# Kernel optimization log

Measured on AMD Instinct MI355X. Metric: run time of the kernel, lower is better.

## Reference

```python
import jax, jax.numpy as jnp
import numpy as np
from jax import lax

NUM_CLS = 58

def _bsign(a):
    # BNN sign: +1 for a >= 0, -1 otherwise
    return jnp.where(a >= 0, 1.0, -1.0).astype(a.dtype)

def _conv(x, w, stride=1):
    return lax.conv_general_dilated(
        x, w, window_strides=(stride, stride), padding='VALID',
        dimension_numbers=('NCHW', 'OIHW', 'NCHW'))

def _binconv(x, w):
    # BinaryConv2d: binarize activations and weights via sign, then conv
    return _conv(_bsign(x), _bsign(w))

def _maxpool(x, k=2, s=2):
    return lax.reduce_window(x, -jnp.inf, lax.max,
                             (1, 1, k, k), (1, 1, s, s), 'VALID')

def setup_inputs() -> dict:
    key = jax.random.key(0)
    ks = jax.random.split(key, 7)
    B = 1024
    x = jax.random.normal(ks[0], (B, 3, 32, 32), dtype=jnp.float32)
    w0 = jax.random.normal(ks[1], (128, 3, 3, 3), dtype=jnp.float32) * 0.1   # float conv
    w1 = jax.random.normal(ks[2], (128, 128, 3, 3), dtype=jnp.float32) * 0.1 # binary conv
    w2 = jax.random.normal(ks[3], (128, 128, 3, 3), dtype=jnp.float32) * 0.1 # binary conv
    w3 = jax.random.normal(ks[4], (128, 128, 3, 3), dtype=jnp.float32) * 0.1 # binary conv
    w4 = jax.random.normal(ks[5], (128, 128, 1, 1), dtype=jnp.float32) * 0.1 # binary 1x1
    w5 = jax.random.normal(ks[6], (NUM_CLS, 128, 1, 1), dtype=jnp.float32) * 0.1  # float 1x1
    return {'x': x, 'w0': w0, 'w1': w1, 'w2': w2, 'w3': w3, 'w4': w4, 'w5': w5}

def reference(x, w0, w1, w2, w3, w4, w5):
    # features
    h = _conv(x, w0)            # [B,128,30,30]
    h = _maxpool(h, 2, 2)       # [B,128,15,15]
    h = _binconv(h, w1)         # [B,128,13,13]
    h = _maxpool(h, 2, 2)       # [B,128,6,6]
    h = _binconv(h, w2)         # [B,128,4,4]
    h = _maxpool(h, 2, 1)       # [B,128,3,3]
    # classifier
    h = _binconv(h, w3)         # [B,128,1,1]
    h = _binconv(h, w4)         # [B,128,1,1]
    h = jax.nn.relu(h)
    h = _conv(h, w5)            # [B,58,1,1]
    return jax.nn.softmax(h, axis=1)
```

## Files before the change

kernel.cpp:

```cpp
#include <hip/hip_runtime.h>
#include <cmath>

#define NUM_CLS 58

typedef _Float16 v8h __attribute__((ext_vector_type(8)));
typedef float v4f __attribute__((ext_vector_type(4)));
union HU { v8h h; uint4 u; };

__global__ __launch_bounds__(256) void prep_all(
    const float* __restrict__ w0, const float* __restrict__ w1,
    const float* __restrict__ w2, const float* __restrict__ w3,
    const float* __restrict__ w4,
    unsigned long long* __restrict__ wb1, unsigned long long* __restrict__ wb2,
    unsigned long long* __restrict__ wb3, unsigned long long* __restrict__ wb4,
    _Float16* __restrict__ bsig, _Float16* __restrict__ babs) {
    int id = blockIdx.x, tid = threadIdx.x;
    int lane = tid & 63, wv = tid >> 6;
    if (id < 384) {
        int layer = id >> 7, oc = id & 127;
        const float* w = layer == 0 ? w1 : (layer == 1 ? w2 : w3);
        unsigned long long* o = layer == 0 ? wb1 : (layer == 1 ? wb2 : wb3);
        __shared__ float s[1152];
        const float* base = w + (size_t)oc * 1152;
        for (int i = tid; i < 1152; i += 256) s[i] = base[i];
        __syncthreads();
        for (int k = wv; k < 9; k += 4) {
            unsigned long long b0 = __ballot(s[lane * 9 + k] >= 0.f);
            unsigned long long b1 = __ballot(s[(lane + 64) * 9 + k] >= 0.f);
            if (lane == 0) { o[(oc * 9 + k) * 2] = b0; o[(oc * 9 + k) * 2 + 1] = b1; }
        }
    } else if (id < 416) {
        int oc = (id - 384) * 4 + wv;
        unsigned long long b0 = __ballot(w4[oc * 128 + lane] >= 0.f);
        unsigned long long b1 = __ballot(w4[oc * 128 + lane + 64] >= 0.f);
        if (lane == 0) { wb4[oc * 2] = b0; wb4[oc * 2 + 1] = b1; }
    } else {
        int nt = (id - 416) * 4 + wv;
        int n = nt * 16 + (lane & 15);
        int k0 = (lane >> 4) * 8;
#pragma unroll
        for (int j = 0; j < 8; j++) {
            int k = k0 + j;
            float v = (k < 27) ? w0[n * 27 + k] : 0.f;
            bsig[(nt * 64 + lane) * 8 + j] = (_Float16)v;
            babs[(nt * 64 + lane) * 8 + j] = (_Float16)fabsf(v);
        }
    }
}

__global__ __launch_bounds__(256, 4) void fused_net(
    const float* __restrict__ x, const float* __restrict__ w0,
    const _Float16* __restrict__ bsigG, const _Float16* __restrict__ babsG,
    const unsigned long long* __restrict__ wb1, const unsigned long long* __restrict__ wb2,
    const unsigned long long* __restrict__ wb3, const unsigned long long* __restrict__ wb4,
    const float* __restrict__ w5, float* __restrict__ out) {
    __shared__ _Float16 xh[3172];
    __shared__ uint4 bfrag[512];
    __shared__ uint4 bfraga[512];
    __shared__ alignas(16) unsigned long long bits1[450];
    __shared__ alignas(16) unsigned long long bits2[72];
    __shared__ unsigned long long bits3[18];
    __shared__ unsigned long long bits4[2];
    __shared__ float r_s[128];
    __shared__ float l_s[NUM_CLS];
    __shared__ float e_s[NUM_CLS];
    __shared__ unsigned int qcnt;
    __shared__ unsigned int queue[256];

    int b = blockIdx.x;
    int tid = threadIdx.x;
    int lane = tid & 63, wave = tid >> 6;
    const float* xb = x + (size_t)b * 3072;

    {
        for (int i = tid; i < 3072; i += 256) {
            int c = i >> 10, rem = i & 1023;
            xh[c * 1057 + (rem >> 5) * 33 + (rem & 31)] = (_Float16)xb[i];
        }
        const uint4* bs4 = (const uint4*)bsigG;
        const uint4* ba4 = (const uint4*)babsG;
        for (int i = tid; i < 512; i += 256) { bfrag[i] = bs4[i]; bfraga[i] = ba4[i]; }
        if (tid == 0) qcnt = 0;

        int k0 = (lane >> 4) * 8;
        int offj[8];
#pragma unroll
        for (int j = 0; j < 8; j++) {
            int k = k0 + j;
            int c = k / 9, r = (k % 9) / 3, q = k % 3;
            offj[j] = c * 1057 + r * 33 + q;
        }
        unsigned short* b1u16 = (unsigned short*)bits1;
        __syncthreads();

        for (int mt = wave; mt < 57; mt += 4) {
            int mg = mt * 16 + (lane & 15);
            int me = mg < 900 ? mg : 899;
            int p = me >> 2, win = me & 3;
            int py = p / 15, px = p - py * 15;
            int base = (py * 2 + (win >> 1)) * 33 + px * 2 + (win & 1);
            v8h a;
#pragma unroll
            for (int j = 0; j < 8; j++)
                a[j] = (k0 + j < 27) ? xh[base + offj[j]] : (_Float16)0.f;
            HU ua; ua.h = a;
            ua.u.x &= 0x7FFF7FFFu; ua.u.y &= 0x7FFF7FFFu;
            ua.u.z &= 0x7FFF7FFFu; ua.u.w &= 0x7FFF7FFFu;
            int myp = mt * 4 + (lane >> 4);
#pragma unroll
            for (int nt = 0; nt < 8; nt++) {
                HU bs; bs.u = bfrag[nt * 64 + lane];
                HU ba; ba.u = bfraga[nt * 64 + lane];
                v4f s  = __builtin_amdgcn_mfma_f32_16x16x32_f16(a,    bs.h, (v4f){0.f,0.f,0.f,0.f}, 0, 0, 0);
                v4f sa = __builtin_amdgcn_mfma_f32_16x16x32_f16(ua.h, ba.h, (v4f){0.f,0.f,0.f,0.f}, 0, 0, 0);
                float bd0 = fmaf(sa[0], 1.1e-3f, 1e-5f);
                float bd1 = fmaf(sa[1], 1.1e-3f, 1e-5f);
                float bd2 = fmaf(sa[2], 1.1e-3f, 1e-5f);
                float bd3 = fmaf(sa[3], 1.1e-3f, 1e-5f);
                unsigned long long mkpos =
                    __ballot(s[0] >= bd0) | __ballot(s[1] >= bd1) |
                    __ballot(s[2] >= bd2) | __ballot(s[3] >= bd3);
                unsigned long long mkunc =
                    (__ballot(fabsf(s[0]) < bd0) | __ballot(fabsf(s[1]) < bd1) |
                     __ballot(fabsf(s[2]) < bd2) | __ballot(fabsf(s[3]) < bd3)) & ~mkpos;
                if ((lane & 15) == 0 && myp < 225)
                    b1u16[myp * 8 + nt] = (unsigned short)(mkpos >> (lane & 48));
                if (__builtin_expect(mkunc != 0ull, 0)) {
                    if (((mkunc >> lane) & 1ull) && myp < 225) {
                        unsigned int qi = atomicAdd(&qcnt, 1u);
                        if (qi < 256) queue[qi] = (unsigned)myp | ((unsigned)(nt * 16 + (lane & 15)) << 8);
                    }
                }
            }
        }
        __syncthreads();
        unsigned int nq = qcnt < 256u ? qcnt : 256u;
        for (unsigned int i = tid; i < nq; i += 256) {
            unsigned int e = queue[i];
            int p = e & 255; int oc = (e >> 8) & 255;
            int py = p / 15, px = p - py * 15;
            bool pos = false;
#pragma unroll
            for (int win = 0; win < 4; win++) {
                int base = (py * 2 + (win >> 1)) * 32 + px * 2 + (win & 1);
                double sd = 0.0;
#pragma unroll
                for (int k = 0; k < 27; k++) {
                    int c = k / 9, r = (k % 9) / 3, q = k % 3;
                    sd += (double)xb[base + c * 1024 + r * 32 + q] * (double)w0[oc * 27 + k];
                }
                pos |= (sd >= 0.0);
            }
            if (pos) atomicOr(&bits1[p * 2 + (oc >> 6)], 1ull << (oc & 63));
        }
    }
    __syncthreads();

    int wave2 = tid >> 6, half = wave2 & 1, pair = wave2 >> 1;
    int oc = half * 64 + lane;

    {
        unsigned long long wr[18];
#pragma unroll
        for (int j = 0; j < 18; j++) wr[j] = wb1[oc * 18 + j];
        const ulonglong2* b1v = (const ulonglong2*)bits1;
        for (int p = pair; p < 36; p += 2) {
            int py = p / 6, px = p % 6;
            int P0 = 0, P1 = 0, P2 = 0, P3 = 0;
#pragma unroll
            for (int yy = 0; yy < 4; yy++) {
                int rb = (2 * py + yy) * 15 + 2 * px;
                ulonglong2 q0 = b1v[rb];
                ulonglong2 q1 = b1v[rb + 1];
                ulonglong2 q2 = b1v[rb + 2];
                ulonglong2 q3 = b1v[rb + 3];
#pragma unroll
                for (int dy = 0; dy < 2; dy++) {
                    int ky = yy - dy;
                    if (ky < 0 || ky > 2) continue;
#pragma unroll
                    for (int kx = 0; kx < 3; kx++) {
                        ulonglong2 qa = kx == 0 ? q0 : (kx == 1 ? q1 : q2);
                        ulonglong2 qb = kx == 0 ? q1 : (kx == 1 ? q2 : q3);
                        int d0 = __popcll(qa.x ^ wr[(ky * 3 + kx) * 2]) +
                                 __popcll(qa.y ^ wr[(ky * 3 + kx) * 2 + 1]);
                        int d1 = __popcll(qb.x ^ wr[(ky * 3 + kx) * 2]) +
                                 __popcll(qb.y ^ wr[(ky * 3 + kx) * 2 + 1]);
                        if (dy == 0) { P0 += d0; P1 += d1; }
                        else         { P2 += d0; P3 += d1; }
                    }
                }
            }
            unsigned long long m = __ballot(P0 <= 576) | __ballot(P1 <= 576) |
                                   __ballot(P2 <= 576) | __ballot(P3 <= 576);
            if (lane == 0) bits2[p * 2 + half] = m;
        }
    }
    __syncthreads();

    {
        unsigned long long wr[18];
#pragma unroll
        for (int j = 0; j < 18; j++) wr[j] = wb2[oc * 18 + j];
        const ulonglong2* b2v = (const ulonglong2*)bits2;
        for (int p = pair; p < 9; p += 2) {
            int py = p / 3, px = p % 3;
            int P4[4];
#pragma unroll
            for (int dy = 0; dy < 2; dy++)
#pragma unroll
                for (int dx = 0; dx < 2; dx++) {
                    int P = 0;
#pragma unroll
                    for (int ky = 0; ky < 3; ky++)
#pragma unroll
                        for (int kx = 0; kx < 3; kx++) {
                            ulonglong2 q = b2v[(py + dy + ky) * 6 + (px + dx + kx)];
                            P += __popcll(q.x ^ wr[(ky * 3 + kx) * 2]);
                            P += __popcll(q.y ^ wr[(ky * 3 + kx) * 2 + 1]);
                        }
                    P4[dy * 2 + dx] = P;
                }
            unsigned long long m = __ballot(P4[0] <= 576) | __ballot(P4[1] <= 576) |
                                   __ballot(P4[2] <= 576) | __ballot(P4[3] <= 576);
            if (lane == 0) bits3[p * 2 + half] = m;
        }
    }
    __syncthreads();

    if (tid < 128) {
        int P = 0;
#pragma unroll
        for (int k = 0; k < 9; k++) {
            P += __popcll(bits3[k * 2] ^ wb3[tid * 18 + k * 2]);
            P += __popcll(bits3[k * 2 + 1] ^ wb3[tid * 18 + k * 2 + 1]);
        }
        unsigned long long m = __ballot(P <= 576);
        if ((tid & 63) == 0) bits4[tid >> 6] = m;
    }
    __syncthreads();
    if (tid < 128) {
        unsigned long long i0 = bits4[0], i1 = bits4[1];
        int v = 128 - 2 * (int)(__popcll(i0 ^ wb4[tid * 2]) + __popcll(i1 ^ wb4[tid * 2 + 1]));
        r_s[tid] = v > 0 ? (float)v : 0.f;
    }
    __syncthreads();
    if (tid < NUM_CLS) {
        float l = 0.f;
#pragma unroll 8
        for (int k = 0; k < 128; k++) l = fmaf(w5[tid * 128 + k], r_s[k], l);
        l_s[tid] = l;
    }
    __syncthreads();
    if (tid < NUM_CLS) {
        float mx = -1e30f;
        for (int k = 0; k < NUM_CLS; k++) mx = fmaxf(mx, l_s[k]);
        e_s[tid] = expf(l_s[tid] - mx);
    }
    __syncthreads();
    if (tid < NUM_CLS) {
        float sum = 0.f;
        for (int k = 0; k < NUM_CLS; k++) sum += e_s[k];
        out[(size_t)b * NUM_CLS + tid] = e_s[tid] / sum;
    }
}

extern "C" void kernel_launch(void* const* d_in, const int* in_sizes, int n_in,
                              void* d_out, int out_size, void* d_ws, size_t ws_size,
                              hipStream_t stream) {
    const float* x  = (const float*)d_in[0];
    const float* w0 = (const float*)d_in[1];
    const float* w1 = (const float*)d_in[2];
    const float* w2 = (const float*)d_in[3];
    const float* w3 = (const float*)d_in[4];
    const float* w4 = (const float*)d_in[5];
    const float* w5 = (const float*)d_in[6];
    float* out = (float*)d_out;

    int B = in_sizes[0] / 3072;

    size_t off = 0;
    auto carve = [&](size_t bytes) {
        void* p = (char*)d_ws + off;
        off += (bytes + 255) & ~(size_t)255;
        return p;
    };
    unsigned long long* wb1 = (unsigned long long*)carve(1152 * 2 * 8);
    unsigned long long* wb2 = (unsigned long long*)carve(1152 * 2 * 8);
    unsigned long long* wb3 = (unsigned long long*)carve(1152 * 2 * 8);
    unsigned long long* wb4 = (unsigned long long*)carve(128 * 2 * 8);
    _Float16* bsig = (_Float16*)carve(8 * 64 * 8 * 2);
    _Float16* babs = (_Float16*)carve(8 * 64 * 8 * 2);
    (void)ws_size; (void)n_in; (void)out_size;

    prep_all<<<418, 256, 0, stream>>>(w0, w1, w2, w3, w4, wb1, wb2, wb3, wb4, bsig, babs);
    fused_net<<<B, 256, 0, stream>>>(x, w0, bsig, babs, wb1, wb2, wb3, wb4, w5, out);
}
```

Baseline: 160.7 us.

## Compute layer-1 binary conv with int8 MFMA instead of XOR-popcount

Layer 1's binary convolution now expands the packed sign bits into ±1 int8 bytes in shared memory and runs it as an int8 MFMA GEMM (16x16x64). The weights are pre-expanded into MFMA fragment layout by the prep kernel. The sign of the full 13x13 output is stored, and the maxpool becomes an OR of four sign bits. This replaces per-lane popcount loops with matrix-core work, at the cost of a larger shared-memory expansion buffer (unioned with stage-0 buffers), extra syncs, and global fragment loads.

```diff
diff --git a/kernel.cpp b/kernel.cpp
--- a/kernel.cpp
+++ b/kernel.cpp
@@ -5,21 +5,23 @@
 
 typedef _Float16 v8h __attribute__((ext_vector_type(8)));
 typedef float v4f __attribute__((ext_vector_type(4)));
+typedef int v4i __attribute__((ext_vector_type(4)));
 union HU { v8h h; uint4 u; };
 
 __global__ __launch_bounds__(256) void prep_all(
     const float* __restrict__ w0, const float* __restrict__ w1,
     const float* __restrict__ w2, const float* __restrict__ w3,
     const float* __restrict__ w4,
-    unsigned long long* __restrict__ wb1, unsigned long long* __restrict__ wb2,
+    unsigned long long* __restrict__ wb2,
     unsigned long long* __restrict__ wb3, unsigned long long* __restrict__ wb4,
-    _Float16* __restrict__ bsig, _Float16* __restrict__ babs) {
+    _Float16* __restrict__ bsig, _Float16* __restrict__ babs,
+    uint4* __restrict__ bw1f) {
     int id = blockIdx.x, tid = threadIdx.x;
     int lane = tid & 63, wv = tid >> 6;
-    if (id < 384) {
+    if (id < 256) {
         int layer = id >> 7, oc = id & 127;
-        const float* w = layer == 0 ? w1 : (layer == 1 ? w2 : w3);
-        unsigned long long* o = layer == 0 ? wb1 : (layer == 1 ? wb2 : wb3);
+        const float* w = layer == 0 ? w2 : w3;
+        unsigned long long* o = layer == 0 ? wb2 : wb3;
         __shared__ float s[1152];
         const float* base = w + (size_t)oc * 1152;
         for (int i = tid; i < 1152; i += 256) s[i] = base[i];
@@ -29,13 +31,13 @@
             unsigned long long b1 = __ballot(s[(lane + 64) * 9 + k] >= 0.f);
             if (lane == 0) { o[(oc * 9 + k) * 2] = b0; o[(oc * 9 + k) * 2 + 1] = b1; }
         }
-    } else if (id < 416) {
-        int oc = (id - 384) * 4 + wv;
+    } else if (id < 288) {
+        int oc = (id - 256) * 4 + wv;
         unsigned long long b0 = __ballot(w4[oc * 128 + lane] >= 0.f);
         unsigned long long b1 = __ballot(w4[oc * 128 + lane + 64] >= 0.f);
         if (lane == 0) { wb4[oc * 2] = b0; wb4[oc * 2 + 1] = b1; }
-    } else {
-        int nt = (id - 416) * 4 + wv;
+    } else if (id < 290) {
+        int nt = (id - 288) * 4 + wv;
         int n = nt * 16 + (lane & 15);
         int k0 = (lane >> 4) * 8;
 #pragma unroll
@@ -45,19 +47,51 @@
             bsig[(nt * 64 + lane) * 8 + j] = (_Float16)v;
             babs[(nt * 64 + lane) * 8 + j] = (_Float16)fabsf(v);
         }
+    } else {
+        int fi = (id - 290) * 256 + tid;
+        int tk = fi >> 9;
+        int rem = fi & 511;
+        int nt = rem >> 6, ln = rem & 63;
+        int oc = nt * 16 + (ln & 15);
+        int tap = tk >> 1, kk = tk & 1;
+        int icb = kk * 64 + (ln >> 4) * 16;
+        const float* wp = w1 + (size_t)oc * 1152 + tap;
+        unsigned int dd[4];
+#pragma unroll
+        for (int q = 0; q < 4; ++q) {
+            unsigned int v = 0;
+#pragma unroll
+            for (int j = 0; j < 4; ++j)
+                v |= (wp[(icb + q * 4 + j) * 9] >= 0.f ? 0x01u : 0xFFu) << (8 * j);
+            dd[q] = v;
+        }
+        uint4 d; d.x = dd[0]; d.y = dd[1]; d.z = dd[2]; d.w = dd[3];
+        bw1f[fi] = d;
     }
 }
+
+union UEXP {
+    struct {
+        _Float16 xh[3172];
+        alignas(16) uint4 bfrag[512];
+        uint4 bfraga[512];
+    } p0;
+    unsigned char expb[225 * 144];
+};
+union BS {
+    alignas(16) unsigned long long bits1[450];
+    unsigned short sgn1[144 * 8];
+};
 
 __global__ __launch_bounds__(256, 4) void fused_net(
     const float* __restrict__ x, const float* __restrict__ w0,
     const _Float16* __restrict__ bsigG, const _Float16* __restrict__ babsG,
-    const unsigned long long* __restrict__ wb1, const unsigned long long* __restrict__ wb2,
+    const uint4* __restrict__ bw1f, const unsigned long long* __restrict__ wb2,
     const unsigned long long* __restrict__ wb3, const unsigned long long* __restrict__ wb4,
     const float* __restrict__ w5, float* __restrict__ out) {
-    __shared__ _Float16 xh[3172];
-    __shared__ uint4 bfrag[512];
-    __shared__ uint4 bfraga[512];
-    __shared__ alignas(16) unsigned long long bits1[450];
+    __shared__ UEXP u;
+    __shared__ BS bs;
+    __shared__ unsigned int lut[16];
     __shared__ alignas(16) unsigned long long bits2[72];
     __shared__ unsigned long long bits3[18];
     __shared__ unsigned long long bits4[2];
@@ -72,14 +106,21 @@
     int lane = tid & 63, wave = tid >> 6;
     const float* xb = x + (size_t)b * 3072;
 
+    if (tid < 16) {
+        unsigned int v = 0;
+#pragma unroll
+        for (int j = 0; j < 4; ++j) v |= (((tid >> j) & 1) ? 0x01u : 0xFFu) << (8 * j);
+        lut[tid] = v;
+    }
+
     {
         for (int i = tid; i < 3072; i += 256) {
             int c = i >> 10, rem = i & 1023;
-            xh[c * 1057 + (rem >> 5) * 33 + (rem & 31)] = (_Float16)xb[i];
+            u.p0.xh[c * 1057 + (rem >> 5) * 33 + (rem & 31)] = (_Float16)xb[i];
         }
         const uint4* bs4 = (const uint4*)bsigG;
         const uint4* ba4 = (const uint4*)babsG;
-        for (int i = tid; i < 512; i += 256) { bfrag[i] = bs4[i]; bfraga[i] = ba4[i]; }
+        for (int i = tid; i < 512; i += 256) { u.p0.bfrag[i] = bs4[i]; u.p0.bfraga[i] = ba4[i]; }
         if (tid == 0) qcnt = 0;
 
         int k0 = (lane >> 4) * 8;
@@ -90,7 +131,7 @@
             int c = k / 9, r = (k % 9) / 3, q = k % 3;
             offj[j] = c * 1057 + r * 33 + q;
         }
-        unsigned short* b1u16 = (unsigned short*)bits1;
+        unsigned short* b1u16 = (unsigned short*)bs.bits1;
         __syncthreads();
 
         for (int mt = wave; mt < 57; mt += 4) {
@@ -102,17 +143,17 @@
             v8h a;
 #pragma unroll
             for (int j = 0; j < 8; j++)
-                a[j] = (k0 + j < 27) ? xh[base + offj[j]] : (_Float16)0.f;
+                a[j] = (k0 + j < 27) ? u.p0.xh[base + offj[j]] : (_Float16)0.f;
             HU ua; ua.h = a;
             ua.u.x &= 0x7FFF7FFFu; ua.u.y &= 0x7FFF7FFFu;
             ua.u.z &= 0x7FFF7FFFu; ua.u.w &= 0x7FFF7FFFu;
             int myp = mt * 4 + (lane >> 4);
 #pragma unroll
             for (int nt = 0; nt < 8; nt++) {
-                HU bs; bs.u = bfrag[nt * 64 + lane];
-                HU ba; ba.u = bfraga[nt * 64 + lane];
-                v4f s  = __builtin_amdgcn_mfma_f32_16x16x32_f16(a,    bs.h, (v4f){0.f,0.f,0.f,0.f}, 0, 0, 0);
-                v4f sa = __builtin_amdgcn_mfma_f32_16x16x32_f16(ua.h, ba.h, (v4f){0.f,0.f,0.f,0.f}, 0, 0, 0);
+                HU bsf; bsf.u = u.p0.bfrag[nt * 64 + lane];
+                HU baf; baf.u = u.p0.bfraga[nt * 64 + lane];
+                v4f s  = __builtin_amdgcn_mfma_f32_16x16x32_f16(a,    bsf.h, (v4f){0.f,0.f,0.f,0.f}, 0, 0, 0);
+                v4f sa = __builtin_amdgcn_mfma_f32_16x16x32_f16(ua.h, baf.h, (v4f){0.f,0.f,0.f,0.f}, 0, 0, 0);
                 float bd0 = fmaf(sa[0], 1.1e-3f, 1e-5f);
                 float bd1 = fmaf(sa[1], 1.1e-3f, 1e-5f);
                 float bd2 = fmaf(sa[2], 1.1e-3f, 1e-5f);
@@ -151,7 +192,68 @@
                 }
                 pos |= (sd >= 0.0);
             }
-            if (pos) atomicOr(&bits1[p * 2 + (oc >> 6)], 1ull << (oc & 63));
+            if (pos) atomicOr(&bs.bits1[p * 2 + (oc >> 6)], 1ull << (oc & 63));
+        }
+    }
+    __syncthreads();
+
+    if (tid < 225) {
+        ulonglong2 bw = ((const ulonglong2*)bs.bits1)[tid];
+        unsigned char* dst = u.expb + tid * 144;
+#pragma unroll
+        for (int c2 = 0; c2 < 2; ++c2) {
+            unsigned long long v = c2 ? bw.y : bw.x;
+#pragma unroll
+            for (int c = 0; c < 4; ++c) {
+                uint4 d;
+                d.x = lut[(v >> (c * 16 +  0)) & 15];
+                d.y = lut[(v >> (c * 16 +  4)) & 15];
+                d.z = lut[(v >> (c * 16 +  8)) & 15];
+                d.w = lut[(v >> (c * 16 + 12)) & 15];
+                *(uint4*)(dst + (c2 * 4 + c) * 16) = d;
+            }
+        }
+    }
+    __syncthreads();
+
+    {
+        int posb144_[9];
+#pragma unroll
+        for (int mt = 0; mt < 9; ++mt) {
+            int w = mt * 16 + (lane & 15);
+            int wy = w / 12, wx = w - wy * 12;
+            posb144_[mt] = (wy * 15 + wx) * 144;
+        }
+        int g16 = (lane >> 4) * 16;
+
+        for (int pass = 0; pass < 2; ++pass) {
+            int nt = wave * 2 + pass;
+            v4i acc[9];
+#pragma unroll
+            for (int mt = 0; mt < 9; ++mt) acc[mt] = (v4i){0, 0, 0, 0};
+#pragma unroll 2
+            for (int tk = 0; tk < 18; ++tk) {
+                int tap = tk >> 1, kk = tk & 1;
+                int tapoff = tap + (tap / 3) * 12;
+                int utk = tapoff * 144 + kk * 64 + g16;
+                uint4 bfr = bw1f[(tk * 8 + nt) * 64 + lane];
+                v4i bf; bf.x = (int)bfr.x; bf.y = (int)bfr.y; bf.z = (int)bfr.z; bf.w = (int)bfr.w;
+#pragma unroll
+                for (int mt = 0; mt < 9; ++mt) {
+                    v4i af = *(const v4i*)(u.expb + (posb144_[mt] + utk));
+                    acc[mt] = __builtin_amdgcn_mfma_i32_16x16x64_i8(af, bf, acc[mt], 0, 0, 0);
+                }
+            }
+#pragma unroll
+            for (int mt = 0; mt < 9; ++mt) {
+#pragma unroll
+                for (int r = 0; r < 4; ++r) {
+                    unsigned long long mm = __ballot(acc[mt][r] >= 0);
+                    if ((lane & 15) == 0)
+                        bs.sgn1[(mt * 16 + (lane >> 4) * 4 + r) * 8 + nt] =
+                            (unsigned short)(mm >> lane);
+                }
+            }
         }
     }
     __syncthreads();
@@ -160,39 +262,13 @@
     int oc = half * 64 + lane;
 
     {
-        unsigned long long wr[18];
-#pragma unroll
-        for (int j = 0; j < 18; j++) wr[j] = wb1[oc * 18 + j];
-        const ulonglong2* b1v = (const ulonglong2*)bits1;
+        int idx = oc >> 4, sh = oc & 15;
         for (int p = pair; p < 36; p += 2) {
             int py = p / 6, px = p % 6;
-            int P0 = 0, P1 = 0, P2 = 0, P3 = 0;
-#pragma unroll
-            for (int yy = 0; yy < 4; yy++) {
-                int rb = (2 * py + yy) * 15 + 2 * px;
-                ulonglong2 q0 = b1v[rb];
-                ulonglong2 q1 = b1v[rb + 1];
-                ulonglong2 q2 = b1v[rb + 2];
-                ulonglong2 q3 = b1v[rb + 3];
-#pragma unroll
-                for (int dy = 0; dy < 2; dy++) {
-                    int ky = yy - dy;
-                    if (ky < 0 || ky > 2) continue;
-#pragma unroll
-                    for (int kx = 0; kx < 3; kx++) {
-                        ulonglong2 qa = kx == 0 ? q0 : (kx == 1 ? q1 : q2);
-                        ulonglong2 qb = kx == 0 ? q1 : (kx == 1 ? q2 : q3);
-                        int d0 = __popcll(qa.x ^ wr[(ky * 3 + kx) * 2]) +
-                                 __popcll(qa.y ^ wr[(ky * 3 + kx) * 2 + 1]);
-                        int d1 = __popcll(qb.x ^ wr[(ky * 3 + kx) * 2]) +
-                                 __popcll(qb.y ^ wr[(ky * 3 + kx) * 2 + 1]);
-                        if (dy == 0) { P0 += d0; P1 += d1; }
-                        else         { P2 += d0; P3 += d1; }
-                    }
-                }
-            }
-            unsigned long long m = __ballot(P0 <= 576) | __ballot(P1 <= 576) |
-                                   __ballot(P2 <= 576) | __ballot(P3 <= 576);
+            int w0i = (2 * py) * 12 + 2 * px;
+            unsigned v = (unsigned)bs.sgn1[w0i * 8 + idx]        | (unsigned)bs.sgn1[(w0i + 1) * 8 + idx]
+                       | (unsigned)bs.sgn1[(w0i + 12) * 8 + idx] | (unsigned)bs.sgn1[(w0i + 13) * 8 + idx];
+            unsigned long long m = __ballot(((v >> sh) & 1u) != 0u);
             if (lane == 0) bits2[p * 2 + half] = m;
         }
     }
@@ -285,14 +361,14 @@
         off += (bytes + 255) & ~(size_t)255;
         return p;
     };
-    unsigned long long* wb1 = (unsigned long long*)carve(1152 * 2 * 8);
     unsigned long long* wb2 = (unsigned long long*)carve(1152 * 2 * 8);
     unsigned long long* wb3 = (unsigned long long*)carve(1152 * 2 * 8);
     unsigned long long* wb4 = (unsigned long long*)carve(128 * 2 * 8);
     _Float16* bsig = (_Float16*)carve(8 * 64 * 8 * 2);
     _Float16* babs = (_Float16*)carve(8 * 64 * 8 * 2);
+    uint4* bw1f = (uint4*)carve(18 * 8 * 64 * 16);
     (void)ws_size; (void)n_in; (void)out_size;
 
-    prep_all<<<418, 256, 0, stream>>>(w0, w1, w2, w3, w4, wb1, wb2, wb3, wb4, bsig, babs);
-    fused_net<<<B, 256, 0, stream>>>(x, w0, bsig, babs, wb1, wb2, wb3, wb4, w5, out);
+    prep_all<<<326, 256, 0, stream>>>(w0, w1, w2, w3, w4, wb2, wb3, wb4, bsig, babs, bw1f);
+    fused_net<<<B, 256, 0, stream>>>(x, w0, bsig, babs, bw1f, wb2, wb3, wb4, w5, out);
 }
```

Result: faster. 150.2 us (-6.5%).
